# Performance work log

Measured on AMD Instinct MI355X. Metric: run time of the kernel, lower is better.

Reference implementation:

```python
import jax, jax.numpy as jnp
import numpy as np

BLOCK_SIZE = 2048
FRAMES = 4096
BASE_RESONANCE = 0.5
MAX_GAIN = 5.0


def fft_convolve(a, b):
    # Linear convolution via zero-padded FFT, truncated to original length
    # (matches the matching-pursuit repo's fft_convolve).
    n = a.shape[-1]
    fa = jnp.fft.rfft(a, n=2 * n, axis=-1)
    fb = jnp.fft.rfft(b, n=2 * n, axis=-1)
    out = jnp.fft.irfft(fa * fb, n=2 * n, axis=-1)
    return out[..., :n]


def setup_inputs() -> dict:
    key = jax.random.key(0)
    ks = jax.random.split(key, 6)
    cp = jax.random.normal(ks[0], (1, BLOCK_SIZE, FRAMES), dtype=jnp.float32)
    w1 = jax.random.uniform(ks[1], (BLOCK_SIZE, BLOCK_SIZE), jnp.float32, -0.01, 0.01)
    w2 = jax.random.uniform(ks[2], (BLOCK_SIZE, BLOCK_SIZE), jnp.float32, -0.01, 0.01)
    audio = jax.random.uniform(ks[3], (BLOCK_SIZE, BLOCK_SIZE), jnp.float32, -0.01, 0.01)
    decays = jax.random.uniform(ks[4], (BLOCK_SIZE,), jnp.float32, 0.001, 0.99)
    gains = jax.random.uniform(ks[5], (BLOCK_SIZE,), jnp.float32, -3.0, 3.0)
    return {"cp": cp, "w1": w1, "w2": w2, "audio": audio, "decays": decays, "gains": gains}


def reference(cp, w1, w2, audio, decays, gains):
    b, c, frames = cp.shape  # b == 1, c == BLOCK_SIZE
    x0 = jnp.maximum(cp, 0.0)  # torch.relu(cp)
    # decay values in (base_resonance, 1): base + sigmoid(decays) * span
    d = BASE_RESONANCE + jax.nn.sigmoid(decays) * (1.0 - BASE_RESONANCE)  # (c,)
    g = jax.nn.sigmoid(gains) * MAX_GAIN  # (c,)

    x = jnp.einsum('ij,bjt->bit', w1, x0)  # mapping @ control_plane
    orig = x

    # decay envelope: log -> cumsum -> exp over frames => d ** (t+1)
    logd = jnp.log(1e-12 + jnp.broadcast_to(d[None, :, None], (b, c, frames)))
    denv = jnp.exp(jnp.cumsum(logd, axis=-1))  # (b, c, frames)

    x = fft_convolve(x, denv)
    x = jnp.einsum('ij,bjt->bit', w2, x) + orig
    cp_out = jnp.tanh(x * g[None, :, None])

    audio_out = jnp.einsum('wj,bjt->bwt', audio, cp_out)  # (b, window, frames)
    audio_out = jnp.transpose(audio_out, (0, 2, 1)).reshape(b, 1, -1)
    return audio_out, cp_out
```

## Files before the change

kernel.cpp:

```cpp
#include <hip/hip_runtime.h>
#include <math.h>

typedef __attribute__((ext_vector_type(8))) short bf16x8;
typedef __attribute__((ext_vector_type(8))) unsigned short u16x8;
typedef __attribute__((ext_vector_type(4))) unsigned short u16x4;
typedef __attribute__((ext_vector_type(4))) float f32x4;
typedef unsigned short u16;

__device__ __forceinline__ u16 f2bf(float f) {
  unsigned u = __builtin_bit_cast(unsigned, f);
  return (u16)((u + 0x7FFFu + ((u >> 16) & 1u)) >> 16);
}

__device__ __forceinline__ void gload16(const u16* g, u16* l) {
  __builtin_amdgcn_global_load_lds((const __attribute__((address_space(1))) void*)g,
                                   (__attribute__((address_space(3))) void*)l, 16, 0, 0);
}

__device__ __forceinline__ void sbar() {
  __builtin_amdgcn_sched_barrier(0);
  __builtin_amdgcn_s_barrier();
  __builtin_amdgcn_sched_barrier(0);
}

#define VMWAIT(n) asm volatile("s_waitcnt vmcnt(" #n ")" ::: "memory")
#define MFMA16(a, b, c) __builtin_amdgcn_mfma_f32_16x16x32_bf16((a), (b), (c), 0, 0, 0)

__device__ __forceinline__ float decay_of(float d) {
  return 1e-12f + 0.5f + 0.5f / (1.0f + expf(-d));
}

__device__ __forceinline__ size_t pack_idx(int nrow, int k) {
  const int bn = nrow >> 7, n16 = (nrow >> 4) & 7, row = nrow & 15;
  const int kt = k >> 6, kh = (k >> 5) & 1, kc = (k >> 3) & 3;
  return ((((size_t)(bn * 32 + kt) * 8 + n16) * 2 + kh) * 4 + kc) * 16 + row;
}

__global__ __launch_bounds__(256) void cvt2_kernel(const float* __restrict__ a,
                                                   const float* __restrict__ b,
                                                   u16* __restrict__ out) {
  const int i = blockIdx.x * 256 + threadIdx.x;
  const float* src = (i < 1048576) ? a : b;
  const int j = (i < 1048576) ? i : i - 1048576;
  const float4 v = ((const float4*)src)[j];
  u16x4 o = { f2bf(v.x), f2bf(v.y), f2bf(v.z), f2bf(v.w) };
  ((u16x4*)out)[i] = o;
}

__global__ __launch_bounds__(256) void audio_pack_kernel(const float* __restrict__ audio,
                                                         u16* __restrict__ pack) {
  const int gid = blockIdx.x * 256 + threadIdx.x;
  const int j = (gid & 255) * 8;
  const int wv = gid >> 8;
  const float4 v0 = *(const float4*)(audio + (size_t)wv * 2048 + j);
  const float4 v1 = *(const float4*)(audio + (size_t)wv * 2048 + j + 4);
  u16x8 o = { f2bf(v0.x), f2bf(v0.y), f2bf(v0.z), f2bf(v0.w),
              f2bf(v1.x), f2bf(v1.y), f2bf(v1.z), f2bf(v1.w) };
  *(u16x8*)(pack + pack_idx(wv, j) * 8) = o;
}

__global__ __launch_bounds__(256) void relu_t_kernel(const float* __restrict__ cp,
                                                     u16* __restrict__ x0p) {
  const int cb = blockIdx.x & 31;
  const int tb = blockIdx.x >> 5;
  __shared__ __attribute__((aligned(16))) float tile[64][65];
  const int tid = threadIdx.x;
  const int r0 = tid >> 4, i4 = (tid & 15) * 4;
  #pragma unroll
  for (int rr = 0; rr < 64; rr += 16) {
    const float4 v = *(const float4*)(cp + (size_t)(cb * 64 + r0 + rr) * 4096 + tb * 64 + i4);
    tile[r0 + rr][i4 + 0] = fmaxf(v.x, 0.f);
    tile[r0 + rr][i4 + 1] = fmaxf(v.y, 0.f);
    tile[r0 + rr][i4 + 2] = fmaxf(v.z, 0.f);
    tile[r0 + rr][i4 + 3] = fmaxf(v.w, 0.f);
  }
  __syncthreads();
  #pragma unroll
  for (int it = 0; it < 2; ++it) {
    const int chunk = it * 256 + tid;
    const int i = chunk >> 3, rp = (chunk & 7) * 8;
    u16x8 o;
    #pragma unroll
    for (int q = 0; q < 8; ++q) o[q] = f2bf(tile[rp + q][i]);
    *(u16x8*)(x0p + pack_idx(tb * 64 + i, cb * 64 + rp) * 8) = o;
  }
}

__global__ __launch_bounds__(128) void iir_partial_kernel(const float* __restrict__ x,
                                                          const float* __restrict__ decays,
                                                          float* __restrict__ L) {
  const int tid = threadIdx.x;
  const int cb = blockIdx.x & 15;
  const int ck = blockIdx.x >> 4;
  const int c0 = cb * 128, t0 = ck * 64;
  __shared__ __attribute__((aligned(16))) float xs[128][65];
  const float dd = decay_of(decays[c0 + tid]);
  #pragma unroll
  for (int it = 0; it < 16; ++it) {
    const int idx = it * 128 + tid;
    const int r = idx >> 4, iv = (idx & 15) * 4;
    const float4 v = *(const float4*)(x + (size_t)(c0 + r) * 4096 + t0 + iv);
    xs[r][iv + 0] = v.x; xs[r][iv + 1] = v.y; xs[r][iv + 2] = v.z; xs[r][iv + 3] = v.w;
  }
  __syncthreads();
  float yv = 0.0f;
  #pragma unroll
  for (int i = 0; i < 64; ++i) yv = dd * (xs[tid][i] + yv);
  L[ck * 2048 + c0 + tid] = yv;
}

__global__ __launch_bounds__(128) void iir_carry_kernel(const float* __restrict__ L,
                                                        const float* __restrict__ decays,
                                                        float* __restrict__ Cin) {
  const int c = blockIdx.x * 128 + threadIdx.x;
  const float dd = decay_of(decays[c]);
  float A = dd;
  #pragma unroll
  for (int p = 0; p < 6; ++p) A = A * A;
  float carry = 0.0f;
  for (int j = 0; j < 64; ++j) {
    Cin[j * 2048 + c] = carry;
    carry = L[j * 2048 + c] + A * carry;
  }
}

__global__ __launch_bounds__(128) void iir_apply_kernel(const float* __restrict__ x,
                                                        const float* __restrict__ decays,
                                                        const float* __restrict__ Cin,
                                                        u16* __restrict__ yp) {
  const int tid = threadIdx.x;
  const int cb = blockIdx.x & 15;
  const int ck = blockIdx.x >> 4;
  const int c0 = cb * 128, t0 = ck * 64;
  __shared__ __attribute__((aligned(16))) float xs[128][65];
  __shared__ __attribute__((aligned(16))) u16 ys[64][136];
  const float dd = decay_of(decays[c0 + tid]);
  const float carry = Cin[ck * 2048 + c0 + tid];
  #pragma unroll
  for (int it = 0; it < 16; ++it) {
    const int idx = it * 128 + tid;
    const int r = idx >> 4, iv = (idx & 15) * 4;
    const float4 v = *(const float4*)(x + (size_t)(c0 + r) * 4096 + t0 + iv);
    xs[r][iv + 0] = v.x; xs[r][iv + 1] = v.y; xs[r][iv + 2] = v.z; xs[r][iv + 3] = v.w;
  }
  __syncthreads();
  float yv = carry;
  #pragma unroll
  for (int i = 0; i < 64; ++i) {
    yv = dd * (xs[tid][i] + yv);
    ys[i][tid] = f2bf(yv);
  }
  __syncthreads();
  #pragma unroll
  for (int it = 0; it < 8; ++it) {
    const int chunk = it * 128 + tid;
    const int i = chunk >> 4, cpv = (chunk & 15) * 8;
    u16x8 v = *(const u16x8*)&ys[i][cpv];
    *(u16x8*)(yp + pack_idx(t0 + i, c0 + cpv) * 8) = v;
  }
}

template <int MODE>
__global__ __launch_bounds__(256, 2) void gemm_bg_kernel(
    const u16* __restrict__ A, const u16* __restrict__ Bp, float* __restrict__ C,
    int N, int K, int xlogn,
    const float* __restrict__ orig, const float* __restrict__ gains,
    u16* __restrict__ CbT) {
  __shared__ __attribute__((aligned(16))) u16 Asb[2][128 * 64];
  const int tid = threadIdx.x;
  const int l = tid & 63, w = tid >> 6;
  const int xc = blockIdx.x & 7, rblk = blockIdx.x >> 3;
  const int xn = xc & ((1 << xlogn) - 1), xm = xc >> xlogn;
  const int bm = xm * 8 + (rblk >> 3);
  const int bn = xn * 8 + (rblk & 7);
  const int nt = K >> 6;

  const int cs = (l & 7) ^ (l >> 3);
  const int rsub = l >> 3;
  const u16* aS[4]; int tO[4];
  #pragma unroll
  for (int u = 0; u < 4; ++u) {
    const int rg = (u * 4 + w) * 8 + rsub;
    aS[u] = A + (size_t)(bm * 128 + rg) * K + cs * 8;
    tO[u] = (u * 4 + w) * 512;
  }

#define STAGEA(buf, tt) do {                                               \
    const long so_ = (long)(tt) * 64;                                      \
    gload16(aS[0] + so_, (buf) + tO[0]); gload16(aS[1] + so_, (buf) + tO[1]); \
    gload16(aS[2] + so_, (buf) + tO[2]); gload16(aS[3] + so_, (buf) + tO[3]); \
  } while (0)

  const int wr = w >> 1, wc = w & 1;
  const int rA0 = wr * 64 + (l & 15);
  const int jk0 = (l >> 4) ^ (l & 7);
  const int jk1 = ((l >> 4) + 4) ^ (l & 7);

  const u16* bBase = Bp + ((size_t)bn * nt * 8 + wc * 4) * 1024 + (size_t)l * 8;

#define LOADB(dst, tt) do {                                                \
    const u16* bp_ = bBase + (size_t)(tt) * 8192;                          \
    dst[0][0] = *(const bf16x8*)(bp_ +    0); dst[0][1] = *(const bf16x8*)(bp_ +  512); \
    dst[1][0] = *(const bf16x8*)(bp_ + 1024); dst[1][1] = *(const bf16x8*)(bp_ + 1536); \
    dst[2][0] = *(const bf16x8*)(bp_ + 2048); dst[2][1] = *(const bf16x8*)(bp_ + 2560); \
    dst[3][0] = *(const bf16x8*)(bp_ + 3072); dst[3][1] = *(const bf16x8*)(bp_ + 3584); \
  } while (0)

#define COMPUTE(Ab, bfr) do {                                              \
    bf16x8 af[4][2];                                                       \
    _Pragma("unroll")                                                      \
    for (int mi = 0; mi < 4; ++mi) {                                       \
      af[mi][0] = *(const bf16x8*)((Ab) + (rA0 + mi * 16) * 64 + jk0 * 8); \
      af[mi][1] = *(const bf16x8*)((Ab) + (rA0 + mi * 16) * 64 + jk1 * 8); \
    }                                                                      \
    __builtin_amdgcn_s_setprio(1);                                         \
    _Pragma("unroll")                                                      \
    for (int mi = 0; mi < 4; ++mi)                                         \
      _Pragma("unroll")                                                    \
      for (int ni = 0; ni < 4; ++ni)                                       \
        acc[mi][ni] = MFMA16(af[mi][0], bfr[ni][0], acc[mi][ni]);          \
    _Pragma("unroll")                                                      \
    for (int mi = 0; mi < 4; ++mi)                                         \
      _Pragma("unroll")                                                    \
      for (int ni = 0; ni < 4; ++ni)                                       \
        acc[mi][ni] = MFMA16(af[mi][1], bfr[ni][1], acc[mi][ni]);          \
    __builtin_amdgcn_s_setprio(0);                                         \
  } while (0)

  f32x4 acc[4][4];
  #pragma unroll
  for (int i = 0; i < 4; ++i)
    #pragma unroll
    for (int j = 0; j < 4; ++j) acc[i][j] = (f32x4){0.f, 0.f, 0.f, 0.f};

  bf16x8 bfE[4][2], bfO[4][2];

  STAGEA((u16*)Asb[0], 0);
  LOADB(bfE, 0);
  STAGEA((u16*)Asb[1], 1);
  VMWAIT(12);
  sbar();

  for (int t = 0; t < nt; t += 2) {
    if (t + 1 < nt) LOADB(bfO, t + 1);
    if (t < nt - 2) { VMWAIT(12); } else { VMWAIT(0); }
    COMPUTE((const u16*)Asb[0], bfE);
    if (t < nt - 2) { VMWAIT(8); } else { VMWAIT(0); }
    sbar();
    if (t + 2 < nt) STAGEA((u16*)Asb[0], t + 2);
    if (t + 2 < nt) LOADB(bfE, t + 2);
    if (t + 1 < nt - 2) { VMWAIT(12); } else { VMWAIT(0); }
    COMPUTE((const u16*)Asb[1], bfO);
    if (t + 1 < nt - 2) { VMWAIT(8); } else { VMWAIT(0); }
    sbar();
    if (t + 3 < nt) STAGEA((u16*)Asb[1], t + 3);
  }
#undef STAGEA
#undef LOADB
#undef COMPUTE

  const int rb = bm * 128 + wr * 64 + ((l >> 4) * 4);
  const int cb = bn * 128 + wc * 64 + (l & 15);
  #pragma unroll
  for (int mi = 0; mi < 4; ++mi) {
    const int row0 = rb + mi * 16;
    float gv[4] = {0.f, 0.f, 0.f, 0.f};
    if (MODE == 1) {
      #pragma unroll
      for (int j = 0; j < 4; ++j) gv[j] = 5.0f / (1.0f + expf(-gains[row0 + j]));
    }
    #pragma unroll
    for (int ni = 0; ni < 4; ++ni) {
      const int col = cb + ni * 16;
      f32x4 v = acc[mi][ni];
      if (MODE == 1) {
        float cpv[4];
        #pragma unroll
        for (int j = 0; j < 4; ++j) {
          float t = v[j] + orig[(size_t)(row0 + j) * N + col];
          cpv[j] = tanhf(t * gv[j]);
          C[(size_t)(row0 + j) * N + col] = cpv[j];
        }
        u16x4 o = { f2bf(cpv[0]), f2bf(cpv[1]), f2bf(cpv[2]), f2bf(cpv[3]) };
        *(u16x4*)(CbT + (size_t)col * 2048 + row0) = o;
      } else {
        #pragma unroll
        for (int j = 0; j < 4; ++j)
          C[(size_t)(row0 + j) * N + col] = v[j];
      }
    }
  }
}

extern "C" void kernel_launch(void* const* d_in, const int* in_sizes, int n_in,
                              void* d_out, int out_size, void* d_ws, size_t ws_size,
                              hipStream_t stream) {
  const float* cp     = (const float*)d_in[0];
  const float* w1     = (const float*)d_in[1];
  const float* w2     = (const float*)d_in[2];
  const float* audio  = (const float*)d_in[3];
  const float* decays = (const float*)d_in[4];
  const float* gains  = (const float*)d_in[5];

  float* out0 = (float*)d_out;
  float* out1 = out0 + (size_t)2048 * 4096;

  char* ws = (char*)d_ws;
  u16*   w1b    = (u16*)(ws);
  u16*   w2b    = (u16*)(ws + 8388608);
  u16*   audp   = (u16*)(ws + 16777216);
  float* orig   = (float*)(ws + 25165824);
  u16*   yp     = (u16*)(ws + 58720256);
  u16*   x0p    = (u16*)(ws + 75497472);
  u16*   cpbT   = x0p;
  float* Lbuf   = (float*)(ws + 75497472);
  float* Cin    = (float*)(ws + 75497472 + 524288);

  cvt2_kernel<<<8192, 256, 0, stream>>>(w1, w2, w1b);
  audio_pack_kernel<<<2048, 256, 0, stream>>>(audio, audp);
  relu_t_kernel<<<2048, 256, 0, stream>>>(cp, x0p);

  gemm_bg_kernel<0><<<512, 256, 0, stream>>>(w1b, x0p, orig, 4096, 2048, 2,
                                             nullptr, nullptr, nullptr);
  iir_partial_kernel<<<1024, 128, 0, stream>>>(orig, decays, Lbuf);
  iir_carry_kernel<<<16, 128, 0, stream>>>(Lbuf, decays, Cin);
  iir_apply_kernel<<<1024, 128, 0, stream>>>(orig, decays, Cin, yp);
  gemm_bg_kernel<1><<<512, 256, 0, stream>>>(w2b, yp, out1, 4096, 2048, 2,
                                             orig, gains, cpbT);
  gemm_bg_kernel<0><<<512, 256, 0, stream>>>(cpbT, audp, out0, 2048, 2048, 1,
                                             nullptr, nullptr, nullptr);
}
```

Before: 197.6 us.

## Deepen GEMM pipeline to four LDS stages with paired barrier periods

```diff
diff --git a/kernel.cpp b/kernel.cpp
--- a/kernel.cpp
+++ b/kernel.cpp
@@ -77,12 +77,14 @@
   __syncthreads();
   #pragma unroll
   for (int it = 0; it < 2; ++it) {
-    const int chunk = it * 256 + tid;
-    const int i = chunk >> 3, rp = (chunk & 7) * 8;
+    const int idx = it * 256 + tid;
+    const int row = idx & 15, fc = idx >> 4;
+    const int n16s = fc >> 3, kcc = fc & 7;
+    const int tl = n16s * 16 + row, cl = kcc * 8;
     u16x8 o;
     #pragma unroll
-    for (int q = 0; q < 8; ++q) o[q] = f2bf(tile[rp + q][i]);
-    *(u16x8*)(x0p + pack_idx(tb * 64 + i, cb * 64 + rp) * 8) = o;
+    for (int q = 0; q < 8; ++q) o[q] = f2bf(tile[cl + q][tl]);
+    *(u16x8*)(x0p + pack_idx(tb * 64 + tl, cb * 64 + cl) * 8) = o;
   }
 }
 
@@ -153,27 +155,28 @@
   __syncthreads();
   #pragma unroll
   for (int it = 0; it < 8; ++it) {
-    const int chunk = it * 128 + tid;
-    const int i = chunk >> 4, cpv = (chunk & 15) * 8;
-    u16x8 v = *(const u16x8*)&ys[i][cpv];
-    *(u16x8*)(yp + pack_idx(t0 + i, c0 + cpv) * 8) = v;
+    const int idx = it * 128 + tid;
+    const int row = idx & 15, fc = idx >> 4;
+    const int n16s = fc >> 4, kcc = fc & 15;
+    const int tl = n16s * 16 + row, cl = kcc * 8;
+    u16x8 v = *(const u16x8*)&ys[tl][cl];
+    *(u16x8*)(yp + pack_idx(t0 + tl, c0 + cl) * 8) = v;
   }
 }
 
 template <int MODE>
-__global__ __launch_bounds__(256, 2) void gemm_bg_kernel(
+__global__ __launch_bounds__(256, 2) void gemm_p2_kernel(
     const u16* __restrict__ A, const u16* __restrict__ Bp, float* __restrict__ C,
     int N, int K, int xlogn,
     const float* __restrict__ orig, const float* __restrict__ gains,
     u16* __restrict__ CbT) {
-  __shared__ __attribute__((aligned(16))) u16 Asb[2][128 * 64];
+  __shared__ __attribute__((aligned(16))) u16 Asb[4][128 * 64];
   const int tid = threadIdx.x;
   const int l = tid & 63, w = tid >> 6;
   const int xc = blockIdx.x & 7, rblk = blockIdx.x >> 3;
   const int xn = xc & ((1 << xlogn) - 1), xm = xc >> xlogn;
   const int bm = xm * 8 + (rblk >> 3);
   const int bn = xn * 8 + (rblk & 7);
-  const int nt = K >> 6;
 
   const int cs = (l & 7) ^ (l >> 3);
   const int rsub = l >> 3;
@@ -184,6 +187,10 @@
     aS[u] = A + (size_t)(bm * 128 + rg) * K + cs * 8;
     tO[u] = (u * 4 + w) * 512;
   }
+  u16* buf0 = (u16*)Asb[0];
+  u16* buf1 = (u16*)Asb[1];
+  u16* buf2 = (u16*)Asb[2];
+  u16* buf3 = (u16*)Asb[3];
 
 #define STAGEA(buf, tt) do {                                               \
     const long so_ = (long)(tt) * 64;                                      \
@@ -196,7 +203,7 @@
   const int jk0 = (l >> 4) ^ (l & 7);
   const int jk1 = ((l >> 4) + 4) ^ (l & 7);
 
-  const u16* bBase = Bp + ((size_t)bn * nt * 8 + wc * 4) * 1024 + (size_t)l * 8;
+  const u16* bBase = Bp + ((size_t)bn * 32 * 8 + wc * 4) * 1024 + (size_t)l * 8;
 
 #define LOADB(dst, tt) do {                                                \
     const u16* bp_ = bBase + (size_t)(tt) * 8192;                          \
@@ -227,37 +234,42 @@
     __builtin_amdgcn_s_setprio(0);                                         \
   } while (0)
 
+#define PERIOD(T, BUFA, BUFB, CUR0, CUR1, NXT0, NXT1) do {                 \
+    const bool m2_ = (T) + 2 < 32, m4_ = (T) + 4 < 32;                     \
+    if (m2_) { LOADB(NXT0, (T) + 2); LOADB(NXT1, (T) + 3); }               \
+    if (m2_) { VMWAIT(32); } else { VMWAIT(8); }                           \
+    COMPUTE(BUFA, CUR0);                                                   \
+    if (m2_) { VMWAIT(24); } else { VMWAIT(0); }                           \
+    COMPUTE(BUFB, CUR1);                                                   \
+    if (m2_) {                                                             \
+      VMWAIT(16);                                                          \
+      sbar();                                                              \
+      if (m4_) { STAGEA(BUFA, (T) + 4); STAGEA(BUFB, (T) + 5); }           \
+    }                                                                      \
+  } while (0)
+
   f32x4 acc[4][4];
   #pragma unroll
   for (int i = 0; i < 4; ++i)
     #pragma unroll
     for (int j = 0; j < 4; ++j) acc[i][j] = (f32x4){0.f, 0.f, 0.f, 0.f};
 
-  bf16x8 bfE[4][2], bfO[4][2];
-
-  STAGEA((u16*)Asb[0], 0);
-  LOADB(bfE, 0);
-  STAGEA((u16*)Asb[1], 1);
-  VMWAIT(12);
+  bf16x8 bP0[4][2], bP1[4][2], bQ0[4][2], bQ1[4][2];
+
+  STAGEA(buf0, 0); STAGEA(buf1, 1);
+  LOADB(bP0, 0);  LOADB(bP1, 1);
+  STAGEA(buf2, 2); STAGEA(buf3, 3);
+  VMWAIT(24);
   sbar();
 
-  for (int t = 0; t < nt; t += 2) {
-    if (t + 1 < nt) LOADB(bfO, t + 1);
-    if (t < nt - 2) { VMWAIT(12); } else { VMWAIT(0); }
-    COMPUTE((const u16*)Asb[0], bfE);
-    if (t < nt - 2) { VMWAIT(8); } else { VMWAIT(0); }
-    sbar();
-    if (t + 2 < nt) STAGEA((u16*)Asb[0], t + 2);
-    if (t + 2 < nt) LOADB(bfE, t + 2);
-    if (t + 1 < nt - 2) { VMWAIT(12); } else { VMWAIT(0); }
-    COMPUTE((const u16*)Asb[1], bfO);
-    if (t + 1 < nt - 2) { VMWAIT(8); } else { VMWAIT(0); }
-    sbar();
-    if (t + 3 < nt) STAGEA((u16*)Asb[1], t + 3);
+  for (int t = 0; t < 32; t += 4) {
+    PERIOD(t,     buf0, buf1, bP0, bP1, bQ0, bQ1);
+    PERIOD(t + 2, buf2, buf3, bQ0, bQ1, bP0, bP1);
   }
 #undef STAGEA
 #undef LOADB
 #undef COMPUTE
+#undef PERIOD
 
   const int rb = bm * 128 + wr * 64 + ((l >> 4) * 4);
   const int cb = bn * 128 + wc * 64 + (l & 15);
@@ -320,13 +332,13 @@
   audio_pack_kernel<<<2048, 256, 0, stream>>>(audio, audp);
   relu_t_kernel<<<2048, 256, 0, stream>>>(cp, x0p);
 
-  gemm_bg_kernel<0><<<512, 256, 0, stream>>>(w1b, x0p, orig, 4096, 2048, 2,
+  gemm_p2_kernel<0><<<512, 256, 0, stream>>>(w1b, x0p, orig, 4096, 2048, 2,
                                              nullptr, nullptr, nullptr);
   iir_partial_kernel<<<1024, 128, 0, stream>>>(orig, decays, Lbuf);
   iir_carry_kernel<<<16, 128, 0, stream>>>(Lbuf, decays, Cin);
   iir_apply_kernel<<<1024, 128, 0, stream>>>(orig, decays, Cin, yp);
-  gemm_bg_kernel<1><<<512, 256, 0, stream>>>(w2b, yp, out1, 4096, 2048, 2,
+  gemm_p2_kernel<1><<<512, 256, 0, stream>>>(w2b, yp, out1, 4096, 2048, 2,
                                              orig, gains, cpbT);
-  gemm_bg_kernel<0><<<512, 256, 0, stream>>>(cpbT, audp, out0, 2048, 2048, 1,
+  gemm_p2_kernel<0><<<512, 256, 0, stream>>>(cpbT, audp, out0, 2048, 2048, 1,
                                              nullptr, nullptr, nullptr);
 }
```

Measured after the change: 217.9 us. +10.3%, slower.
